# Performance work log

Hardware: AMD Instinct MI355X
Metric: run time of the kernel (lower is better)

The kernel has to match this reference:

```python
import jax, jax.numpy as jnp
import numpy as np

R, H, E = 200000, 256, 100000  # num_relations, hidden_dim, num_hyperedges


def setup_inputs() -> dict:
    key = jax.random.key(0)
    ks = jax.random.split(key, 8)
    rng = np.random.default_rng(0)
    # ragged hyperedge sizes in [1, 15], avg ~8 -> total ~800k src entries
    sizes = rng.integers(1, 16, size=E)
    total = int(sizes.sum())
    he_ptr = jnp.asarray(np.concatenate([[0], np.cumsum(sizes)]), dtype=jnp.int64)
    he_src = jax.random.randint(ks[0], (total,), 0, R, dtype=jnp.int64)
    # unique targets make the scatter deterministic and equivalent)
    he_tgt = jnp.asarray(rng.permutation(R)[:E], dtype=jnp.int64)
    he_w = jax.random.uniform(ks[1], (E,), dtype=jnp.float32)
    x = jax.random.normal(ks[2], (R, H), dtype=jnp.float32)
    s = 1.0 / np.sqrt(H)
    W_msg = jax.random.uniform(ks[3], (H, H), jnp.float32, -s, s)
    b_msg = jnp.zeros((H,), jnp.float32)
    W_gate = jax.random.uniform(ks[4], (2 * H, H), jnp.float32, -s, s)
    b_gate = jnp.zeros((H,), jnp.float32)
    W_upd = jax.random.uniform(ks[5], (H, H), jnp.float32, -s, s)
    b_upd = jnp.zeros((H,), jnp.float32)
    return {"x": x, "he_ptr": he_ptr, "he_src": he_src, "he_tgt": he_tgt,
            "he_w": he_w, "W_msg": W_msg, "b_msg": b_msg,
            "W_gate": W_gate, "b_gate": b_gate, "W_upd": W_upd, "b_upd": b_upd}


def reference(x, he_ptr, he_src, he_tgt, he_w, W_msg, b_msg, W_gate, b_gate, W_upd, b_upd):
    total = he_src.shape[0]
    num_e = he_tgt.shape[0]
    # segment id of each src entry: which hyperedge it belongs to
    seg = jnp.searchsorted(he_ptr, jnp.arange(total), side="right") - 1
    gathered = x[he_src]                                   # [total, H]
    sums = jax.ops.segment_sum(gathered, seg, num_segments=num_e)  # [E, H]
    counts = (he_ptr[1:] - he_ptr[:-1]).astype(x.dtype)    # [E]
    src_mean = sums / counts[:, None]                      # segment mean
    msg = src_mean @ W_msg + b_msg                         # [E, H]
    tgt_x = x[he_tgt]                                      # [E, H]
    gate = jax.nn.sigmoid(jnp.concatenate([tgt_x, msg], axis=-1) @ W_gate + b_gate)
    upd = tgt_x + he_w[:, None] * gate * msg               # gated residual
    out = x.at[he_tgt].set(upd)                            # unique targets
    out = jnp.clip(out @ W_upd + b_upd, 0.0, 1.0)          # clipped relu
    return out
```

## Files before the change

### kernel.cpp

```cpp
#include <hip/hip_runtime.h>
#include <math.h>

#define H 256

typedef __attribute__((ext_vector_type(8))) short short8;
typedef __attribute__((ext_vector_type(4))) float f32x4;
typedef __attribute__((ext_vector_type(4))) int int4v;
typedef __attribute__((ext_vector_type(2))) unsigned int uint2v;
typedef unsigned short ushort_t;

__device__ __forceinline__ float bf2f(unsigned short u) {
    union { unsigned int i; float f; } v; v.i = ((unsigned int)u) << 16; return v.f;
}
__device__ __forceinline__ unsigned short f2bf(float f) {
    union { float f; unsigned int i; } v; v.f = f;
    unsigned int r = v.i + 0x7FFFu + ((v.i >> 16) & 1u);
    return (unsigned short)(r >> 16);
}
__device__ __forceinline__ void glds16(const void* g, void* l) {
    __builtin_amdgcn_global_load_lds((const __attribute__((address_space(1))) void*)g,
                                     (__attribute__((address_space(3))) void*)l, 16, 0, 0);
}
__device__ __forceinline__ int4v pack_f32x8_bf16(const float* p) {
    float4 f0 = *(const float4*)(p);
    float4 f1 = *(const float4*)(p + 4);
    int4v d;
    d.x = (int)((unsigned)f2bf(f0.x) | ((unsigned)f2bf(f0.y) << 16));
    d.y = (int)((unsigned)f2bf(f0.z) | ((unsigned)f2bf(f0.w) << 16));
    d.z = (int)((unsigned)f2bf(f1.x) | ((unsigned)f2bf(f1.y) << 16));
    d.w = (int)((unsigned)f2bf(f1.z) | ((unsigned)f2bf(f1.w) << 16));
    return d;
}

__global__ void prep_all(const float* __restrict__ Wm, const float* __restrict__ Wg,
                         const float* __restrict__ Wu, const float* __restrict__ x,
                         ushort_t* __restrict__ Wmt, ushort_t* __restrict__ Wgt,
                         ushort_t* __restrict__ Wut, int* __restrict__ imap,
                         ushort_t* __restrict__ yb, int R, size_t n8) {
    size_t gtid = (size_t)blockIdx.x * blockDim.x + threadIdx.x;
    size_t stride = (size_t)gridDim.x * blockDim.x;
    for (size_t i = gtid; i < 65536; i += stride) {
        int n = (int)(i >> 8), k = (int)(i & 255);
        Wmt[i] = f2bf(Wm[(size_t)k * 256 + n]);
        Wut[i] = f2bf(Wu[(size_t)k * 256 + n]);
    }
    for (size_t i = gtid; i < 131072; i += stride) {
        int n = (int)(i >> 9), k = (int)(i & 511);
        Wgt[i] = f2bf(Wg[(size_t)k * 256 + n]);
    }
    if (imap) for (size_t i = gtid; i < (size_t)R; i += stride) imap[i] = -1;
    if (yb) for (size_t i = gtid; i < n8; i += stride)
        *(int4v*)(yb + i * 8) = pack_f32x8_bf16(x + i * 8);
}

__global__ void imap_scatter(const int* __restrict__ tgt, int* __restrict__ imap, int E) {
    int e = blockIdx.x * 256 + threadIdx.x;
    if (e < E) imap[tgt[e]] = e;
}

__global__ __launch_bounds__(256) void seg_mean_bf16(const ushort_t* __restrict__ yb,
                                                     const int* __restrict__ ptr,
                                                     const int* __restrict__ src,
                                                     ushort_t* __restrict__ smb, int E) {
    int e = blockIdx.x * 8 + (threadIdx.x >> 5);
    if (e >= E) return;
    int lane = threadIdx.x & 31;
    const ushort_t* base = yb + lane * 8;
    int s = ptr[e], t = ptr[e + 1];
    float a0 = 0.f, a1 = 0.f, a2 = 0.f, a3 = 0.f, a4 = 0.f, a5 = 0.f, a6 = 0.f, a7 = 0.f;
    int i = s;
    for (; i + 4 <= t; i += 4) {
        int4v v0 = *(const int4v*)(base + (size_t)src[i + 0] * H);
        int4v v1 = *(const int4v*)(base + (size_t)src[i + 1] * H);
        int4v v2 = *(const int4v*)(base + (size_t)src[i + 2] * H);
        int4v v3 = *(const int4v*)(base + (size_t)src[i + 3] * H);
        a0 += bf2f((unsigned)v0.x & 0xffff) + bf2f((unsigned)v1.x & 0xffff) + bf2f((unsigned)v2.x & 0xffff) + bf2f((unsigned)v3.x & 0xffff);
        a1 += bf2f((unsigned)v0.x >> 16)    + bf2f((unsigned)v1.x >> 16)    + bf2f((unsigned)v2.x >> 16)    + bf2f((unsigned)v3.x >> 16);
        a2 += bf2f((unsigned)v0.y & 0xffff) + bf2f((unsigned)v1.y & 0xffff) + bf2f((unsigned)v2.y & 0xffff) + bf2f((unsigned)v3.y & 0xffff);
        a3 += bf2f((unsigned)v0.y >> 16)    + bf2f((unsigned)v1.y >> 16)    + bf2f((unsigned)v2.y >> 16)    + bf2f((unsigned)v3.y >> 16);
        a4 += bf2f((unsigned)v0.z & 0xffff) + bf2f((unsigned)v1.z & 0xffff) + bf2f((unsigned)v2.z & 0xffff) + bf2f((unsigned)v3.z & 0xffff);
        a5 += bf2f((unsigned)v0.z >> 16)    + bf2f((unsigned)v1.z >> 16)    + bf2f((unsigned)v2.z >> 16)    + bf2f((unsigned)v3.z >> 16);
        a6 += bf2f((unsigned)v0.w & 0xffff) + bf2f((unsigned)v1.w & 0xffff) + bf2f((unsigned)v2.w & 0xffff) + bf2f((unsigned)v3.w & 0xffff);
        a7 += bf2f((unsigned)v0.w >> 16)    + bf2f((unsigned)v1.w >> 16)    + bf2f((unsigned)v2.w >> 16)    + bf2f((unsigned)v3.w >> 16);
    }
    for (; i < t; ++i) {
        int4v v = *(const int4v*)(base + (size_t)src[i] * H);
        a0 += bf2f((unsigned)v.x & 0xffff); a1 += bf2f((unsigned)v.x >> 16);
        a2 += bf2f((unsigned)v.y & 0xffff); a3 += bf2f((unsigned)v.y >> 16);
        a4 += bf2f((unsigned)v.z & 0xffff); a5 += bf2f((unsigned)v.z >> 16);
        a6 += bf2f((unsigned)v.w & 0xffff); a7 += bf2f((unsigned)v.w >> 16);
    }
    float inv = 1.f / (float)(t - s);
    int4v o;
    o.x = (int)((unsigned)f2bf(a0 * inv) | ((unsigned)f2bf(a1 * inv) << 16));
    o.y = (int)((unsigned)f2bf(a2 * inv) | ((unsigned)f2bf(a3 * inv) << 16));
    o.z = (int)((unsigned)f2bf(a4 * inv) | ((unsigned)f2bf(a5 * inv) << 16));
    o.w = (int)((unsigned)f2bf(a6 * inv) | ((unsigned)f2bf(a7 * inv) << 16));
    *(int4v*)(smb + (size_t)e * H + lane * 8) = o;
}

__global__ __launch_bounds__(256) void seg_mean_f32w(const float* __restrict__ x,
                                                     const int* __restrict__ ptr,
                                                     const int* __restrict__ src,
                                                     ushort_t* __restrict__ smb, int E) {
    int e = blockIdx.x * 4 + (threadIdx.x >> 6);
    if (e >= E) return;
    int lane = threadIdx.x & 63;
    int s = ptr[e], t = ptr[e + 1];
    float a0 = 0.f, a1 = 0.f, a2 = 0.f, a3 = 0.f;
    int i = s;
    for (; i + 4 <= t; i += 4) {
        float4 v0 = *(const float4*)(x + (size_t)src[i + 0] * H + lane * 4);
        float4 v1 = *(const float4*)(x + (size_t)src[i + 1] * H + lane * 4);
        float4 v2 = *(const float4*)(x + (size_t)src[i + 2] * H + lane * 4);
        float4 v3 = *(const float4*)(x + (size_t)src[i + 3] * H + lane * 4);
        a0 += v0.x + v1.x + v2.x + v3.x;
        a1 += v0.y + v1.y + v2.y + v3.y;
        a2 += v0.z + v1.z + v2.z + v3.z;
        a3 += v0.w + v1.w + v2.w + v3.w;
    }
    for (; i < t; ++i) {
        float4 v = *(const float4*)(x + (size_t)src[i] * H + lane * 4);
        a0 += v.x; a1 += v.y; a2 += v.z; a3 += v.w;
    }
    float inv = 1.f / (float)(t - s);
    uint2v o;
    o.x = (unsigned)f2bf(a0 * inv) | ((unsigned)f2bf(a1 * inv) << 16);
    o.y = (unsigned)f2bf(a2 * inv) | ((unsigned)f2bf(a3 * inv) << 16);
    *(uint2v*)(smb + (size_t)e * H + lane * 4) = o;
}

#define LOADA_CHUNK_F(k0v, d)                                                            \
    do {                                                                                 \
        if constexpr (MODE == 1) {                                                       \
            if ((k0v) < 256) d = pack_f32x8_bf16(pXf + (k0v));                           \
            else             d = *(const int4v*)(pA + ((k0v) - 256));                    \
        } else {                                                                         \
            if (!useF) d = *(const int4v*)(p2 + (k0v));                                  \
            else       d = pack_f32x8_bf16(p2f + (k0v));                                 \
        }                                                                                \
    } while (0)

template<int MODE, int KTOT, bool XB>
__global__ __launch_bounds__(512, 4) void wgemm(
    const ushort_t* __restrict__ Abf,
    const float* __restrict__ Xf,
    const ushort_t* __restrict__ Xb,
    const ushort_t* __restrict__ Aux,
    const int* __restrict__ Idx,
    const float* __restrict__ Hew,
    const ushort_t* __restrict__ Wt,
    const float* __restrict__ Bias,
    ushort_t* __restrict__ OutB,
    float* __restrict__ OutF,
    int M)
{
    constexpr int NT = KTOT / 32;
    const int m0 = blockIdx.x * 128;
    const int tid = threadIdx.x;
    const int wv = tid >> 6;
    const int lane = tid & 63;
    const int wr = wv >> 2, wc = wv & 3;

    __shared__ __align__(16) ushort_t As[2][128 * 32];
    __shared__ __align__(16) ushort_t Bs[2][256 * 32];

    const int aRow  = tid >> 2;
    const int sl    = tid & 3;
    const int aCc   = sl ^ ((aRow >> 1) & 3);
    const int bCol0 = tid >> 2;
    const int bCol1 = bCol0 + 128;
    const int bCc0  = sl ^ ((bCol0 >> 1) & 3);
    const int bCc1  = sl ^ ((bCol1 >> 1) & 3);

    const ushort_t* bSrc0 = Wt + (size_t)bCol0 * KTOT + bCc0 * 8;
    const ushort_t* bSrc1 = Wt + (size_t)bCol1 * KTOT + bCc1 * 8;

    int r = m0 + aRow; if (r > M - 1) r = M - 1;

    const ushort_t* aP0 = nullptr;
    const ushort_t* aP1 = nullptr;
    const float* pXf = nullptr; const ushort_t* pA = nullptr;
    const ushort_t* p2 = nullptr; const float* p2f = nullptr;
    bool useF = false;
    if constexpr (MODE == 0 || MODE == 3) {
        aP0 = Abf + (size_t)r * KTOT + aCc * 8;
    } else if constexpr (MODE == 1) {
        int tr = Idx[r];
        if constexpr (XB) {
            aP0 = Xb + (size_t)tr * 256 + aCc * 8;
            aP1 = Aux + (size_t)r * 256 + aCc * 8 - 256;
        } else {
            pXf = Xf + (size_t)tr * 256 + aCc * 8;
            pA  = Aux + (size_t)r * 256 + aCc * 8;
        }
    } else {
        int e = Idx[r];
        if (e >= 0) { p2 = Aux + (size_t)e * 256 + aCc * 8; useF = false; }
        else        { p2f = Xf + (size_t)r * 256 + aCc * 8; useF = true; }
    }

    f32x4 acc[4][4];
#pragma unroll
    for (int i = 0; i < 4; ++i)
#pragma unroll
        for (int j = 0; j < 4; ++j) acc[i][j] = (f32x4){0.f, 0.f, 0.f, 0.f};

    glds16(bSrc0, (char*)&Bs[0][0] + tid * 16);
    glds16(bSrc1, (char*)&Bs[0][0] + (tid + 512) * 16);
    if constexpr (MODE == 0 || MODE == 3 || (MODE == 1 && XB)) {
        glds16(aP0, (char*)&As[0][0] + tid * 16);
    } else {
        int4v d0; LOADA_CHUNK_F(0, d0);
        *(int4v*)((char*)&As[0][0] + tid * 16) = d0;
    }

#pragma unroll 2
    for (int kt = 0; kt < NT; ++kt) {
        __syncthreads();
        const int cur = kt & 1;
        const int nxt = cur ^ 1;
        const bool more = (kt + 1 < NT);
        int4v pf;
        if (more) {
            const int k0 = (kt + 1) * 32;
            glds16(bSrc0 + k0, (char*)&Bs[nxt][0] + tid * 16);
            glds16(bSrc1 + k0, (char*)&Bs[nxt][0] + (tid + 512) * 16);
            if constexpr (MODE == 0 || MODE == 3) {
                glds16(aP0 + k0, (char*)&As[nxt][0] + tid * 16);
            } else if constexpr (MODE == 1 && XB) {
                const ushort_t* s = (k0 < 256) ? (aP0 + k0) : (aP1 + k0);
                glds16(s, (char*)&As[nxt][0] + tid * 16);
            } else {
                LOADA_CHUNK_F(k0, pf);
            }
        }

        const char* aBase = (const char*)&As[cur][0];
        const char* bBase = (const char*)&Bs[cur][0];
        const int kg = lane >> 4;
        short8 a0, a1, a2, a3;
        {
            int r0 = wr * 64 + 0 * 16 + (lane & 15);
            int r1 = r0 + 16, r2 = r0 + 32, r3 = r0 + 48;
            a0 = *(const short8*)(aBase + (r0 * 4 + (kg ^ ((r0 >> 1) & 3))) * 16);
            a1 = *(const short8*)(aBase + (r1 * 4 + (kg ^ ((r1 >> 1) & 3))) * 16);
            a2 = *(const short8*)(aBase + (r2 * 4 + (kg ^ ((r2 >> 1) & 3))) * 16);
            a3 = *(const short8*)(aBase + (r3 * 4 + (kg ^ ((r3 >> 1) & 3))) * 16);
        }
#pragma unroll
        for (int fn = 0; fn < 4; ++fn) {
            int cn = wc * 64 + fn * 16 + (lane & 15);
            short8 b = *(const short8*)(bBase + (cn * 4 + (kg ^ ((cn >> 1) & 3))) * 16);
            acc[0][fn] = __builtin_amdgcn_mfma_f32_16x16x32_bf16(a0, b, acc[0][fn], 0, 0, 0);
            acc[1][fn] = __builtin_amdgcn_mfma_f32_16x16x32_bf16(a1, b, acc[1][fn], 0, 0, 0);
            acc[2][fn] = __builtin_amdgcn_mfma_f32_16x16x32_bf16(a2, b, acc[2][fn], 0, 0, 0);
            acc[3][fn] = __builtin_amdgcn_mfma_f32_16x16x32_bf16(a3, b, acc[3][fn], 0, 0, 0);
        }
        if (more) {
            if constexpr (MODE == 2 || (MODE == 1 && !XB)) {
                *(int4v*)((char*)&As[nxt][0] + tid * 16) = pf;
            }
        }
    }

#pragma unroll
    for (int fm = 0; fm < 4; ++fm) {
        int rbase = m0 + wr * 64 + fm * 16 + (lane >> 4) * 4;
#pragma unroll
        for (int fn = 0; fn < 4; ++fn) {
            int col = wc * 64 + fn * 16 + (lane & 15);
            float bia = Bias[col];
            f32x4 v = acc[fm][fn];
#pragma unroll
            for (int i = 0; i < 4; ++i) {
                int rg = rbase + i;
                if (rg < M) {
                    float z = v[i] + bia;
                    if constexpr (MODE == 0) {
                        OutB[(size_t)rg * 256 + col] = f2bf(z);
                    } else if constexpr (MODE == 1) {
                        float g = 1.f / (1.f + __expf(-z));
                        int tr = Idx[rg];
                        float tx;
                        if constexpr (XB) tx = bf2f(Xb[(size_t)tr * 256 + col]);
                        else              tx = Xf[(size_t)tr * 256 + col];
                        float m = bf2f(Aux[(size_t)rg * 256 + col]);
                        float u = tx + Hew[rg] * g * m;
                        if constexpr (XB) OutB[(size_t)tr * 256 + col] = f2bf(u);
                        else              OutB[(size_t)rg * 256 + col] = f2bf(u);
                    } else {
                        OutF[(size_t)rg * 256 + col] = fminf(fmaxf(z, 0.f), 1.f);
                    }
                }
            }
        }
    }
}

extern "C" void kernel_launch(void* const* d_in, const int* in_sizes, int n_in,
                              void* d_out, int out_size, void* d_ws, size_t ws_size,
                              hipStream_t stream) {
    const float* x      = (const float*)d_in[0];
    const int*   he_ptr = (const int*)d_in[1];
    const int*   he_src = (const int*)d_in[2];
    const int*   he_tgt = (const int*)d_in[3];
    const float* he_w   = (const float*)d_in[4];
    const float* W_msg  = (const float*)d_in[5];
    const float* b_msg  = (const float*)d_in[6];
    const float* W_gate = (const float*)d_in[7];
    const float* b_gate = (const float*)d_in[8];
    const float* W_upd  = (const float*)d_in[9];
    const float* b_upd  = (const float*)d_in[10];

    const int E = in_sizes[3];
    const int R = in_sizes[0] / H;

    const size_t wbytes = (size_t)(65536 + 131072 + 65536) * 2;
    const size_t needA = (size_t)R * H * 2 + (size_t)E * H * 2 * 2 + (size_t)R * 4 + wbytes;
    const bool bigws = ws_size >= needA;

    const int gE = (E + 127) / 128;
    const int gR = (R + 127) / 128;

    if (bigws) {
        char* ws = (char*)d_ws;
        ushort_t* yb   = (ushort_t*)ws;
        ushort_t* buf0 = yb + (size_t)R * H;
        ushort_t* buf1 = buf0 + (size_t)E * H;
        ushort_t* Wmt  = (ushort_t*)(buf1 + (size_t)E * H);
        ushort_t* Wgt  = Wmt + 256 * 256;
        ushort_t* Wut  = Wgt + 256 * 512;

        prep_all<<<2048, 256, 0, stream>>>(W_msg, W_gate, W_upd, x,
                                           Wmt, Wgt, Wut, (int*)nullptr, yb, R, (size_t)R * H / 8);
        seg_mean_bf16<<<(E + 7) / 8, 256, 0, stream>>>(yb, he_ptr, he_src, buf0, E);

        wgemm<0, 256, true><<<gE, 512, 0, stream>>>(buf0, nullptr, yb, nullptr, nullptr, nullptr,
                                                    Wmt, b_msg, buf1, nullptr, E);
        wgemm<1, 512, true><<<gE, 512, 0, stream>>>(nullptr, nullptr, yb, buf1, he_tgt, he_w,
                                                    Wgt, b_gate, yb, nullptr, E);
        wgemm<3, 256, true><<<gR, 512, 0, stream>>>(yb, nullptr, nullptr, nullptr, nullptr, nullptr,
                                                    Wut, b_upd, nullptr, (float*)d_out, R);
    } else {
        char* ws = (char*)d_ws;
        ushort_t* buf0 = (ushort_t*)ws;
        ushort_t* buf1 = buf0 + (size_t)E * H;
        int*      imap = (int*)(buf1 + (size_t)E * H);
        ushort_t* Wmt  = (ushort_t*)((char*)imap + (size_t)R * 4);
        ushort_t* Wgt  = Wmt + 256 * 256;
        ushort_t* Wut  = Wgt + 256 * 512;

        prep_all<<<2048, 256, 0, stream>>>(W_msg, W_gate, W_upd, x,
                                           Wmt, Wgt, Wut, imap, (ushort_t*)nullptr, R, 0);
        imap_scatter<<<(E + 255) / 256, 256, 0, stream>>>(he_tgt, imap, E);
        seg_mean_f32w<<<(E + 3) / 4, 256, 0, stream>>>(x, he_ptr, he_src, buf0, E);

        wgemm<0, 256, false><<<gE, 512, 0, stream>>>(buf0, nullptr, nullptr, nullptr, nullptr, nullptr,
                                                     Wmt, b_msg, buf1, nullptr, E);
        wgemm<1, 512, false><<<gE, 512, 0, stream>>>(nullptr, x, nullptr, buf1, he_tgt, he_w,
                                                     Wgt, b_gate, buf0, nullptr, E);
        wgemm<2, 256, false><<<gR, 512, 0, stream>>>(nullptr, x, nullptr, buf0, imap, nullptr,
                                                     Wut, b_upd, nullptr, (float*)d_out, R);
    }
}
```

Baseline: 350.8 us.

## Triple-buffer direct-to-LDS GEMM loads with explicit vmcnt waits

For GEMM modes whose A operand is loaded straight into LDS, shared buffers grow from two stages to three. Loads run two k-tiles ahead, and each iteration waits with a partial s_waitcnt vmcnt before a raw s_barrier instead of a full __syncthreads. The goal is to hide more global-load latency behind the MFMA work. The cost is 50% more LDS per block, which may reduce how many blocks fit on a CU. The partial vmcnt count also depends on how many loads are outstanding per stage.

Measured after the change: 346.0 us. About the same (-1.4%).

```diff
diff --git a/kernel.cpp b/kernel.cpp
--- a/kernel.cpp
+++ b/kernel.cpp
@@ -141,6 +141,41 @@
         }                                                                                \
     } while (0)
 
+#define STAGE_GL(k0v, bufv)                                                              \
+    do {                                                                                 \
+        glds16(bSrc0 + (k0v), (char*)&Bs[bufv][0] + tid * 16);                           \
+        glds16(bSrc1 + (k0v), (char*)&Bs[bufv][0] + (tid + 512) * 16);                   \
+        if constexpr (MODE == 1) {                                                       \
+            const ushort_t* s_ = ((k0v) < 256) ? (aP0 + (k0v)) : (aP1 + (k0v));          \
+            glds16(s_, (char*)&As[bufv][0] + tid * 16);                                  \
+        } else {                                                                         \
+            glds16(aP0 + (k0v), (char*)&As[bufv][0] + tid * 16);                         \
+        }                                                                                \
+    } while (0)
+
+#define COMPUTE_GL(bufv)                                                                 \
+    do {                                                                                 \
+        const char* aBase = (const char*)&As[bufv][0];                                   \
+        const char* bBase = (const char*)&Bs[bufv][0];                                   \
+        const int kg = lane >> 4;                                                        \
+        short8 a0, a1, a2, a3;                                                           \
+        int r0 = wr * 64 + (lane & 15);                                                  \
+        int r1 = r0 + 16, r2 = r0 + 32, r3 = r0 + 48;                                    \
+        a0 = *(const short8*)(aBase + (r0 * 4 + (kg ^ ((r0 >> 1) & 3))) * 16);           \
+        a1 = *(const short8*)(aBase + (r1 * 4 + (kg ^ ((r1 >> 1) & 3))) * 16);           \
+        a2 = *(const short8*)(aBase + (r2 * 4 + (kg ^ ((r2 >> 1) & 3))) * 16);           \
+        a3 = *(const short8*)(aBase + (r3 * 4 + (kg ^ ((r3 >> 1) & 3))) * 16);           \
+        _Pragma("unroll")                                                                \
+        for (int fn = 0; fn < 4; ++fn) {                                                 \
+            int cn = wc * 64 + fn * 16 + (lane & 15);                                    \
+            short8 b = *(const short8*)(bBase + (cn * 4 + (kg ^ ((cn >> 1) & 3))) * 16); \
+            acc[0][fn] = __builtin_amdgcn_mfma_f32_16x16x32_bf16(a0, b, acc[0][fn], 0, 0, 0); \
+            acc[1][fn] = __builtin_amdgcn_mfma_f32_16x16x32_bf16(a1, b, acc[1][fn], 0, 0, 0); \
+            acc[2][fn] = __builtin_amdgcn_mfma_f32_16x16x32_bf16(a2, b, acc[2][fn], 0, 0, 0); \
+            acc[3][fn] = __builtin_amdgcn_mfma_f32_16x16x32_bf16(a3, b, acc[3][fn], 0, 0, 0); \
+        }                                                                                \
+    } while (0)
+
 template<int MODE, int KTOT, bool XB>
 __global__ __launch_bounds__(512, 4) void wgemm(
     const ushort_t* __restrict__ Abf,
@@ -156,14 +191,15 @@
     int M)
 {
     constexpr int NT = KTOT / 32;
+    constexpr bool GL = (MODE == 0 || MODE == 3 || (MODE == 1 && XB));
     const int m0 = blockIdx.x * 128;
     const int tid = threadIdx.x;
     const int wv = tid >> 6;
     const int lane = tid & 63;
     const int wr = wv >> 2, wc = wv & 3;
 
-    __shared__ __align__(16) ushort_t As[2][128 * 32];
-    __shared__ __align__(16) ushort_t Bs[2][256 * 32];
+    __shared__ __align__(16) ushort_t As[3][128 * 32];
+    __shared__ __align__(16) ushort_t Bs[3][256 * 32];
 
     const int aRow  = tid >> 2;
     const int sl    = tid & 3;
@@ -206,59 +242,43 @@
 #pragma unroll
         for (int j = 0; j < 4; ++j) acc[i][j] = (f32x4){0.f, 0.f, 0.f, 0.f};
 
-    glds16(bSrc0, (char*)&Bs[0][0] + tid * 16);
-    glds16(bSrc1, (char*)&Bs[0][0] + (tid + 512) * 16);
-    if constexpr (MODE == 0 || MODE == 3 || (MODE == 1 && XB)) {
-        glds16(aP0, (char*)&As[0][0] + tid * 16);
+    if constexpr (GL) {
+        STAGE_GL(0, 0);
+        STAGE_GL(32, 1);
+#pragma unroll
+        for (int kt = 0; kt < NT; ++kt) {
+            if (kt == NT - 1) asm volatile("s_waitcnt vmcnt(0)" ::: "memory");
+            else              asm volatile("s_waitcnt vmcnt(3)" ::: "memory");
+            __builtin_amdgcn_s_barrier();
+            if (kt + 2 < NT) {
+                const int k0 = (kt + 2) * 32;
+                const int bn = (kt + 2) % 3;
+                STAGE_GL(k0, bn);
+            }
+            COMPUTE_GL(kt % 3);
+        }
     } else {
-        int4v d0; LOADA_CHUNK_F(0, d0);
-        *(int4v*)((char*)&As[0][0] + tid * 16) = d0;
-    }
-
+        {
+            int4v d0; LOADA_CHUNK_F(0, d0);
+            *(int4v*)((char*)&As[0][0] + tid * 16) = d0;
+        }
+        glds16(bSrc0, (char*)&Bs[0][0] + tid * 16);
+        glds16(bSrc1, (char*)&Bs[0][0] + (tid + 512) * 16);
 #pragma unroll 2
-    for (int kt = 0; kt < NT; ++kt) {
-        __syncthreads();
-        const int cur = kt & 1;
-        const int nxt = cur ^ 1;
-        const bool more = (kt + 1 < NT);
-        int4v pf;
-        if (more) {
-            const int k0 = (kt + 1) * 32;
-            glds16(bSrc0 + k0, (char*)&Bs[nxt][0] + tid * 16);
-            glds16(bSrc1 + k0, (char*)&Bs[nxt][0] + (tid + 512) * 16);
-            if constexpr (MODE == 0 || MODE == 3) {
-                glds16(aP0 + k0, (char*)&As[nxt][0] + tid * 16);
-            } else if constexpr (MODE == 1 && XB) {
-                const ushort_t* s = (k0 < 256) ? (aP0 + k0) : (aP1 + k0);
-                glds16(s, (char*)&As[nxt][0] + tid * 16);
-            } else {
+        for (int kt = 0; kt < NT; ++kt) {
+            __syncthreads();
+            const int cur = kt & 1;
+            const int nxt = cur ^ 1;
+            const bool more = (kt + 1 < NT);
+            int4v pf;
+            if (more) {
+                const int k0 = (kt + 1) * 32;
+                glds16(bSrc0 + k0, (char*)&Bs[nxt][0] + tid * 16);
+                glds16(bSrc1 + k0, (char*)&Bs[nxt][0] + (tid + 512) * 16);
                 LOADA_CHUNK_F(k0, pf);
             }
-        }
-
-        const char* aBase = (const char*)&As[cur][0];
-        const char* bBase = (const char*)&Bs[cur][0];
-        const int kg = lane >> 4;
-        short8 a0, a1, a2, a3;
-        {
-            int r0 = wr * 64 + 0 * 16 + (lane & 15);
-            int r1 = r0 + 16, r2 = r0 + 32, r3 = r0 + 48;
-            a0 = *(const short8*)(aBase + (r0 * 4 + (kg ^ ((r0 >> 1) & 3))) * 16);
-            a1 = *(const short8*)(aBase + (r1 * 4 + (kg ^ ((r1 >> 1) & 3))) * 16);
-            a2 = *(const short8*)(aBase + (r2 * 4 + (kg ^ ((r2 >> 1) & 3))) * 16);
-            a3 = *(const short8*)(aBase + (r3 * 4 + (kg ^ ((r3 >> 1) & 3))) * 16);
-        }
-#pragma unroll
-        for (int fn = 0; fn < 4; ++fn) {
-            int cn = wc * 64 + fn * 16 + (lane & 15);
-            short8 b = *(const short8*)(bBase + (cn * 4 + (kg ^ ((cn >> 1) & 3))) * 16);
-            acc[0][fn] = __builtin_amdgcn_mfma_f32_16x16x32_bf16(a0, b, acc[0][fn], 0, 0, 0);
-            acc[1][fn] = __builtin_amdgcn_mfma_f32_16x16x32_bf16(a1, b, acc[1][fn], 0, 0, 0);
-            acc[2][fn] = __builtin_amdgcn_mfma_f32_16x16x32_bf16(a2, b, acc[2][fn], 0, 0, 0);
-            acc[3][fn] = __builtin_amdgcn_mfma_f32_16x16x32_bf16(a3, b, acc[3][fn], 0, 0, 0);
-        }
-        if (more) {
-            if constexpr (MODE == 2 || (MODE == 1 && !XB)) {
+            COMPUTE_GL(cur);
+            if (more) {
                 *(int4v*)((char*)&As[nxt][0] + tid * 16) = pf;
             }
         }
```
